# Performance work log

Hardware: AMD Instinct MI355X
Metric: run time of the kernel (lower is better)

## Reference

```python
import jax, jax.numpy as jnp
import numpy as np

N_NODES = 100000
N_EDGES = 3200000
HID = 32
N_LAYERS = 3
EDGE_DIM = 2
NODE_IN = 2          # [P, Q]
V_DIM = 2            # [V_mag, V_angle]
VH = V_DIM + HID     # 34, per-node feature fed to the GNN layer
MSG_IN = 2 * VH + EDGE_DIM   # 70
UPD_IN = VH + HID            # 66


def setup_inputs() -> dict:
    key = jax.random.key(0)
    ks = jax.random.split(key, 16)
    s = lambda *sh: 1.0 / np.sqrt(sh[-2]) if len(sh) >= 2 else 0.0
    inp = {
        "P_Q_inj": jax.random.normal(ks[0], (N_NODES, NODE_IN), dtype=jnp.float32),
        "senders": jax.random.randint(ks[1], (N_EDGES,), 0, N_NODES, dtype=jnp.int32),
        "receivers": jax.random.randint(ks[2], (N_EDGES,), 0, N_NODES, dtype=jnp.int32),
        "edge_features": jax.random.normal(ks[3], (N_EDGES, EDGE_DIM), dtype=jnp.float32),
        "edge_mask": jax.random.uniform(ks[4], (N_EDGES,), dtype=jnp.float32),
        # input embedding Dense(hidden_dim)
        "W_in": jax.random.normal(ks[5], (NODE_IN, HID), dtype=jnp.float32) * s(NODE_IN, HID),
        "b_in": jnp.zeros((HID,), dtype=jnp.float32),
        # per-layer params (flax compact loop -> distinct params per layer), stacked on axis 0
        "W_msg": jax.random.normal(ks[6], (N_LAYERS, MSG_IN, HID), dtype=jnp.float32) * s(MSG_IN, HID),
        "b_msg": jnp.zeros((N_LAYERS, HID), dtype=jnp.float32),
        "W_upd": jax.random.normal(ks[7], (N_LAYERS, UPD_IN, HID), dtype=jnp.float32) * s(UPD_IN, HID),
        "b_upd": jnp.zeros((N_LAYERS, HID), dtype=jnp.float32),
        "W_delta": jax.random.normal(ks[8], (N_LAYERS, HID, V_DIM), dtype=jnp.float32) * s(HID, V_DIM),
        "b_delta": jnp.zeros((N_LAYERS, V_DIM), dtype=jnp.float32),
    }
    return inp


def _layer(v, senders, receivers, edge_features, edge_mask, W_msg, b_msg, W_upd, b_upd):
    # v: [N, VH] node features. Gather sender/receiver feats, edge-wise MLP message,
    # soft mask, scatter-sum to receivers, then dense node update.
    msg_in = jnp.concatenate([v[senders], v[receivers], edge_features], axis=-1)  # [E, 70]
    m = jax.nn.relu(msg_in @ W_msg + b_msg)                                       # [E, H]
    m = m * edge_mask[:, None]
    agg = jax.ops.segment_sum(m, receivers, num_segments=v.shape[0])              # [N, H]
    v_out = jnp.concatenate([v, agg], axis=-1) @ W_upd + b_upd                    # [N, H]
    return v_out


def reference(P_Q_inj, senders, receivers, edge_features, edge_mask,
              W_in, b_in, W_msg, b_msg, W_upd, b_upd, W_delta, b_delta):
    V_pred = jnp.zeros_like(P_Q_inj).at[:, 0].set(1.0)   # [N, 2]
    h = P_Q_inj @ W_in + b_in                            # [N, H]
    for l in range(N_LAYERS):
        v_input = jnp.concatenate([V_pred, h], axis=-1)  # [N, 34]
        v_out = _layer(v_input, senders, receivers, edge_features, edge_mask,
                       W_msg[l], b_msg[l], W_upd[l], b_upd[l])
        h = jax.nn.relu(v_out)
        delta_V = h @ W_delta[l] + b_delta[l]
        V_pred = V_pred + delta_V
    return V_pred
```

## Files before the change

kernel.cpp:

```cpp
#include <hip/hip_runtime.h>
#include <hip/hip_fp16.h>

#define NN 100000
#define NE 3200000
#define NB 1563
#define NBLK ((NN + 255) / 256)
#define CHUNK 8192
#define NCH 391
#define CAP 4096
#define NKEY 8192

typedef float f32x4 __attribute__((ext_vector_type(4)));
typedef unsigned int u32x4 __attribute__((ext_vector_type(4)));

__device__ __forceinline__ float2 h2f2(unsigned int u) {
  __half2 h;
  *reinterpret_cast<unsigned int*>(&h) = u;
  return __half22float2(h);
}
__device__ __forceinline__ unsigned int f2h2(float x, float y) {
  __half2 h = __floats2half2_rn(x, y);
  return *reinterpret_cast<unsigned int*>(&h);
}


__global__ __launch_bounds__(1024) void k_hist(const int* __restrict__ recv, int* __restrict__ histmat) {
  __shared__ int h[NB];
  int t = threadIdx.x, c = blockIdx.x;
  for (int i = t; i < NB; i += 1024) h[i] = 0;
  __syncthreads();
  int start = c * CHUNK;
  int end = min(start + CHUNK, NE);
  for (int i = start + t; i < end; i += 1024)
    atomicAdd(&h[__builtin_nontemporal_load(recv + i) >> 6], 1);
  __syncthreads();
  for (int i = t; i < NB; i += 1024) histmat[c * NB + i] = h[i];
}


__global__ __launch_bounds__(256) void k_scanA(const int* __restrict__ histmat, int* __restrict__ total) {
  int b = blockIdx.x * 256 + threadIdx.x;
  if (b >= NB) return;
  int s = 0;
#pragma unroll 4
  for (int c = 0; c < NCH; c++) s += histmat[c * NB + b];
  total[b] = s;
}


__global__ __launch_bounds__(256) void k_scanB(const int* __restrict__ total, int* __restrict__ boff) {
  __shared__ int ps[256];
  int t = threadIdx.x;
  const int PER = (NB + 255) / 256;
  int v[PER];
  int s = 0;
#pragma unroll
  for (int k = 0; k < PER; k++) {
    int i = t * PER + k;
    v[k] = (i < NB) ? total[i] : 0;
    s += v[k];
  }
  ps[t] = s;
  __syncthreads();
  for (int o = 1; o < 256; o <<= 1) {
    int x = (t >= o) ? ps[t - o] : 0;
    __syncthreads();
    ps[t] += x;
    __syncthreads();
  }
  int run = (t > 0) ? ps[t - 1] : 0;
#pragma unroll
  for (int k = 0; k < PER; k++) {
    int i = t * PER + k;
    if (i < NB) {
      boff[i] = run;
      run += v[k];
    }
  }
  if (t == 255) boff[NB] = ps[255];
}


__global__ __launch_bounds__(256) void k_scanC(int* __restrict__ histmat, const int* __restrict__ boff) {
  int b = blockIdx.x * 256 + threadIdx.x;
  if (b >= NB) return;
  int run = boff[b];
#pragma unroll 4
  for (int c = 0; c < NCH; c++) {
    int v = histmat[c * NB + b];
    histmat[c * NB + b] = run;
    run += v;
  }
}


__global__ __launch_bounds__(1024) void k_scat(const int* __restrict__ send, const int* __restrict__ recv,
                                               const float2* __restrict__ ef, const float* __restrict__ mask,
                                               const int* __restrict__ boffc, float4* __restrict__ sorted) {
  __shared__ float4 stg[CHUNK];
  __shared__ unsigned short bkt[CHUNK];
  __shared__ int ofs[NB];
  __shared__ int cur[NB];
  __shared__ int wsum[16];
  int t = threadIdx.x, c = blockIdx.x;
  int start = c * CHUNK;
  int end = min(start + CHUNK, NE);
  int len = end - start;
  for (int i = t; i < NB; i += 1024) cur[i] = 0;
  __syncthreads();
  for (int i = start + t; i < end; i += 1024)
    atomicAdd(&cur[__builtin_nontemporal_load(recv + i) >> 6], 1);
  __syncthreads();
  int v0 = (2 * t < NB) ? cur[2 * t] : 0;
  int v1 = (2 * t + 1 < NB) ? cur[2 * t + 1] : 0;
  int s = v0 + v1;
  int lane = t & 63, wid = t >> 6;
  for (int o = 1; o < 64; o <<= 1) {
    int x = __shfl_up(s, o);
    if (lane >= o) s += x;
  }
  if (lane == 63) wsum[wid] = s;
  __syncthreads();
  if (wid == 0) {
    int ws = (lane < 16) ? wsum[lane] : 0;
    for (int o = 1; o < 16; o <<= 1) {
      int x = __shfl_up(ws, o);
      if (lane >= o) ws += x;
    }
    if (lane < 16) wsum[lane] = ws;
  }
  __syncthreads();
  int excl = s - v0 - v1 + ((wid > 0) ? wsum[wid - 1] : 0);
  __syncthreads();
  if (2 * t < NB) {
    cur[2 * t] = excl;
    ofs[2 * t] = boffc[c * NB + 2 * t] - excl;
  }
  if (2 * t + 1 < NB) {
    cur[2 * t + 1] = excl + v0;
    ofs[2 * t + 1] = boffc[c * NB + 2 * t + 1] - (excl + v0);
  }
  __syncthreads();
  for (int i = start + t; i < end; i += 1024) {
    int r = recv[i];
    int b = r >> 6;
    int p = atomicAdd(&cur[b], 1);
    float2 e2 = ef[i];
    float4 vv;
    vv.x = __int_as_float((send[i] << 6) | (r & 63));
    vv.y = e2.x;
    vv.z = e2.y;
    vv.w = mask[i];
    stg[p] = vv;
    bkt[p] = (unsigned short)b;
  }
  __syncthreads();
  for (int p = t; p < len; p += 1024) {
    int b = bkt[p];
    sorted[ofs[b] + p] = stg[p];
  }
}


__global__ __launch_bounds__(256) void k_bsort(const int* __restrict__ boff, float4* __restrict__ sorted,
                                               int* __restrict__ row_off) {
  __shared__ int cnt[NKEY];
  __shared__ int part[256];
  __shared__ float4 stg[CAP];
  int t = threadIdx.x, b = blockIdx.x;
  int base = boff[b], end = boff[b + 1];
  int Eb = end - base;
  int n0 = b * 64;
  for (int i = t; i < NKEY; i += 256) cnt[i] = 0;
  __syncthreads();
  for (int e = base + t; e < end; e += 256) {
    int pk = __float_as_int(sorted[e].x);
    int key = ((pk & 63) << 7) | (pk >> 16);
    atomicAdd(&cnt[key], 1);
  }
  __syncthreads();
  int s = 0;
#pragma unroll
  for (int k = 0; k < 32; k++) s += cnt[t * 32 + k];
  part[t] = s;
  __syncthreads();
  for (int o = 1; o < 256; o <<= 1) {
    int x = (t >= o) ? part[t - o] : 0;
    __syncthreads();
    part[t] += x;
    __syncthreads();
  }
  int run = part[t] - s;
#pragma unroll
  for (int k = 0; k < 32; k++) {
    int c = cnt[t * 32 + k];
    cnt[t * 32 + k] = run;
    run += c;
  }
  __syncthreads();
  if (t < 64) {
    int n = n0 + t;
    if (n < NN) row_off[n] = base + cnt[t << 7];
  }
  if (b == NB - 1 && t == 0) row_off[NN] = end;
  __syncthreads();
  for (int e = base + t; e < end; e += 256) {
    float4 r = sorted[e];
    int pk = __float_as_int(r.x);
    int key = ((pk & 63) << 7) | (pk >> 16);
    int p = atomicAdd(&cnt[key], 1);
    stg[p] = r;
  }
  __syncthreads();
  for (int i = t; i < Eb; i += 256) sorted[base + i] = stg[i];
}


__global__ __launch_bounds__(256) void k_init(const float2* __restrict__ PQ,
                                              const float* __restrict__ Win, const float* __restrict__ bin,
                                              const float* __restrict__ Wm, const float* __restrict__ bm,
                                              float* __restrict__ h, __half* __restrict__ a,
                                              float* __restrict__ bp, float2* __restrict__ Vp) {
  int n = blockIdx.x * 256 + threadIdx.x;
  if (n >= NN) return;
  float2 pq = PQ[n];
  float hh[32];
#pragma unroll
  for (int j = 0; j < 32; j++) hh[j] = fmaf(pq.x, Win[j], fmaf(pq.y, Win[32 + j], bin[j]));
  float4* h4 = (float4*)(h + (size_t)n * 32);
#pragma unroll
  for (int j = 0; j < 8; j++) h4[j] = make_float4(hh[4*j], hh[4*j+1], hh[4*j+2], hh[4*j+3]);
  Vp[n] = make_float2(1.0f, 0.0f);
  float av[32], bv[32];
#pragma unroll
  for (int j = 0; j < 32; j++) { av[j] = Wm[j]; bv[j] = Wm[34 * 32 + j] + bm[j]; }
#pragma unroll 1
  for (int k = 0; k < 32; k++) {
    float hk = hh[k];
#pragma unroll
    for (int j = 0; j < 32; j++) {
      av[j] = fmaf(hk, Wm[(2 + k) * 32 + j], av[j]);
      bv[j] = fmaf(hk, Wm[(36 + k) * 32 + j], bv[j]);
    }
  }
  u32x4* dst = (u32x4*)(a + (size_t)n * 32);
#pragma unroll
  for (int g = 0; g < 4; g++) {
    u32x4 p;
    p.x = f2h2(av[g*8+0], av[g*8+1]);
    p.y = f2h2(av[g*8+2], av[g*8+3]);
    p.z = f2h2(av[g*8+4], av[g*8+5]);
    p.w = f2h2(av[g*8+6], av[g*8+7]);
    dst[g] = p;
  }
  float4* b4 = (float4*)(bp + (size_t)n * 32);
#pragma unroll
  for (int j = 0; j < 8; j++) b4[j] = make_float4(bv[4*j], bv[4*j+1], bv[4*j+2], bv[4*j+3]);
}


__global__ __launch_bounds__(256) void k_edge(const __half* __restrict__ a, const float* __restrict__ bp,
                                              const int* __restrict__ row_off, const f32x4* __restrict__ sorted,
                                              const float* __restrict__ Wm, float* __restrict__ agg) {
  int t = threadIdx.x;
  int n = blockIdx.x * 64 + (t >> 2);
  if (n >= NN) return;
  int ch = (t & 3) * 8;
  const float* wr = Wm + 68 * 32 + ch;
  float w0[8], w1[8];
#pragma unroll
  for (int j = 0; j < 8; j++) { w0[j] = wr[j]; w1[j] = wr[32 + j]; }
  const float4 bna = *(const float4*)(bp + (size_t)n * 32 + ch);
  const float4 bnb = *(const float4*)(bp + (size_t)n * 32 + ch + 4);
  float bn[8] = {bna.x, bna.y, bna.z, bna.w, bnb.x, bnb.y, bnb.z, bnb.w};
  float acc[8] = {0.f, 0.f, 0.f, 0.f, 0.f, 0.f, 0.f, 0.f};
  const __half* abase = a + ch;
  int e0 = row_off[n], e1 = row_off[n + 1];
  f32x4 r0 = {0,0,0,0}, r1 = {0,0,0,0}, r2 = {0,0,0,0};
  u32x4 gA = {0,0,0,0}, gB = {0,0,0,0};
  if (e0 < e1)     r0 = __builtin_nontemporal_load(sorted + e0);
  if (e0 + 1 < e1) r1 = __builtin_nontemporal_load(sorted + e0 + 1);
  if (e0 + 2 < e1) r2 = __builtin_nontemporal_load(sorted + e0 + 2);
  if (e0 < e1)     gA = *(const u32x4*)(abase + (size_t)(__float_as_int(r0.x) >> 6) * 32);
  if (e0 + 1 < e1) gB = *(const u32x4*)(abase + (size_t)(__float_as_int(r1.x) >> 6) * 32);
  for (int e = e0; e < e1; ++e) {
    f32x4 rc = r0;
    u32x4 q = gA;
    r0 = r1; r1 = r2; gA = gB;
    if (e + 3 < e1) r2 = __builtin_nontemporal_load(sorted + e + 3);
    if (e + 2 < e1)
      gB = *(const u32x4*)(abase + (size_t)(__float_as_int(r1.x) >> 6) * 32);
    float c0 = rc.y, c1 = rc.z, mk = rc.w;
    float2 f0 = h2f2(q.x), f1 = h2f2(q.y), f2 = h2f2(q.z), f3 = h2f2(q.w);
    float av[8] = {f0.x, f0.y, f1.x, f1.y, f2.x, f2.y, f3.x, f3.y};
#pragma unroll
    for (int j = 0; j < 8; j++)
      acc[j] = fmaf(fmaxf(av[j] + fmaf(c0, w0[j], fmaf(c1, w1[j], bn[j])), 0.f), mk, acc[j]);
  }
  float* gp = agg + (size_t)n * 32 + ch;
  *(float4*)gp       = make_float4(acc[0], acc[1], acc[2], acc[3]);
  *(float4*)(gp + 4) = make_float4(acc[4], acc[5], acc[6], acc[7]);
}


__global__ __launch_bounds__(256) void k_node(const float* __restrict__ agg,
                                              const float* __restrict__ Wu, const float* __restrict__ bu,
                                              const float* __restrict__ Wd, const float* __restrict__ bd,
                                              const float* __restrict__ Wm, const float* __restrict__ bm,
                                              float* __restrict__ h, __half* __restrict__ a,
                                              float* __restrict__ bp, float2* __restrict__ Vp,
                                              float2* __restrict__ out, int last) {
  int n = blockIdx.x * 256 + threadIdx.x;
  if (n >= NN) return;
  float2 vp = Vp[n];
  float v0 = vp.x, v1 = vp.y;
  float hh[32], ag[32];
  const float4* h4 = (const float4*)(h + (size_t)n * 32);
  const float4* g4 = (const float4*)(agg + (size_t)n * 32);
#pragma unroll
  for (int jj = 0; jj < 8; jj++) {
    float4 x = h4[jj];
    hh[4*jj] = x.x; hh[4*jj+1] = x.y; hh[4*jj+2] = x.z; hh[4*jj+3] = x.w;
    float4 y = g4[jj];
    ag[4*jj] = y.x; ag[4*jj+1] = y.y; ag[4*jj+2] = y.z; ag[4*jj+3] = y.w;
  }
  float vo[32];
#pragma unroll
  for (int j = 0; j < 32; j++) vo[j] = fmaf(v0, Wu[j], fmaf(v1, Wu[32 + j], bu[j]));
#pragma unroll 1
  for (int k = 0; k < 32; k++) {
    float hk = hh[k], ak = ag[k];
#pragma unroll
    for (int j = 0; j < 32; j++) {
      vo[j] = fmaf(hk, Wu[(2 + k) * 32 + j], vo[j]);
      vo[j] = fmaf(ak, Wu[(34 + k) * 32 + j], vo[j]);
    }
  }
#pragma unroll
  for (int j = 0; j < 32; j++) hh[j] = fmaxf(vo[j], 0.0f);
  float d0 = bd[0], d1 = bd[1];
#pragma unroll 1
  for (int k = 0; k < 32; k++) {
    d0 = fmaf(hh[k], Wd[2 * k], d0);
    d1 = fmaf(hh[k], Wd[2 * k + 1], d1);
  }
  v0 += d0;
  v1 += d1;
  if (last) {
    out[n] = make_float2(v0, v1);
    return;
  }
  Vp[n] = make_float2(v0, v1);
  float4* hw4 = (float4*)(h + (size_t)n * 32);
#pragma unroll
  for (int jj = 0; jj < 8; jj++) hw4[jj] = make_float4(hh[4*jj], hh[4*jj+1], hh[4*jj+2], hh[4*jj+3]);
  float av[32], bv[32];
#pragma unroll
  for (int j = 0; j < 32; j++) {
    av[j] = fmaf(v0, Wm[j], v1 * Wm[32 + j]);
    bv[j] = fmaf(v0, Wm[34 * 32 + j], fmaf(v1, Wm[35 * 32 + j], bm[j]));
  }
#pragma unroll 1
  for (int k = 0; k < 32; k++) {
    float hk = hh[k];
#pragma unroll
    for (int j = 0; j < 32; j++) {
      av[j] = fmaf(hk, Wm[(2 + k) * 32 + j], av[j]);
      bv[j] = fmaf(hk, Wm[(36 + k) * 32 + j], bv[j]);
    }
  }
  u32x4* dst = (u32x4*)(a + (size_t)n * 32);
#pragma unroll
  for (int g = 0; g < 4; g++) {
    u32x4 p;
    p.x = f2h2(av[g*8+0], av[g*8+1]);
    p.y = f2h2(av[g*8+2], av[g*8+3]);
    p.z = f2h2(av[g*8+4], av[g*8+5]);
    p.w = f2h2(av[g*8+6], av[g*8+7]);
    dst[g] = p;
  }
  float4* b4 = (float4*)(bp + (size_t)n * 32);
#pragma unroll
  for (int jj = 0; jj < 8; jj++) b4[jj] = make_float4(bv[4*jj], bv[4*jj+1], bv[4*jj+2], bv[4*jj+3]);
}


extern "C" void kernel_launch(void* const* d_in, const int* in_sizes, int n_in,
                              void* d_out, int out_size, void* d_ws, size_t ws_size,
                              hipStream_t stream) {
  const float* PQ   = (const float*)d_in[0];
  const int*   send = (const int*)d_in[1];
  const int*   recv = (const int*)d_in[2];
  const float* ef   = (const float*)d_in[3];
  const float* mask = (const float*)d_in[4];
  const float* Win  = (const float*)d_in[5];
  const float* bin  = (const float*)d_in[6];
  const float* Wmsg = (const float*)d_in[7];
  const float* bmsg = (const float*)d_in[8];
  const float* Wupd = (const float*)d_in[9];
  const float* bupd = (const float*)d_in[10];
  const float* Wdel = (const float*)d_in[11];
  const float* bdel = (const float*)d_in[12];
  float2* out = (float2*)d_out;

  char* w = (char*)d_ws;
  auto alloc = [&](size_t bytes) {
    char* p = w;
    w += (bytes + 255) & ~(size_t)255;
    return p;
  };
  float4* sorted = (float4*)alloc((size_t)NE * 16);
  int* histmat = (int*)alloc((size_t)NCH * NB * 4);
  int* total   = (int*)alloc((size_t)NB * 4);
  int* boff    = (int*)alloc(((size_t)NB + 1) * 4);
  int* row_off = (int*)alloc(((size_t)NN + 1) * 4);
  float* h    = (float*)alloc((size_t)NN * 32 * 4);
  __half* a   = (__half*)alloc((size_t)NN * 32 * 2);
  float* bp   = (float*)alloc((size_t)NN * 32 * 4);
  float* agg  = (float*)alloc((size_t)NN * 32 * 4);
  float2* Vp  = (float2*)alloc((size_t)NN * 8);

  k_hist<<<NCH, 1024, 0, stream>>>(recv, histmat);
  k_scanA<<<(NB + 255) / 256, 256, 0, stream>>>(histmat, total);
  k_scanB<<<1, 256, 0, stream>>>(total, boff);
  k_scanC<<<(NB + 255) / 256, 256, 0, stream>>>(histmat, boff);
  k_scat<<<NCH, 1024, 0, stream>>>(send, recv, (const float2*)ef, mask, histmat, sorted);
  k_bsort<<<NB, 256, 0, stream>>>(boff, sorted, row_off);

  k_init<<<NBLK, 256, 0, stream>>>((const float2*)PQ, Win, bin, Wmsg, bmsg, h, a, bp, Vp);

  for (int l = 0; l < 3; l++) {
    int last = (l == 2) ? 1 : 0;
    int lnext = (l + 1) % 3;
    k_edge<<<NB, 256, 0, stream>>>(a, bp, row_off, (const f32x4*)sorted, Wmsg + l * 70 * 32, agg);
    k_node<<<NBLK, 256, 0, stream>>>(agg, Wupd + l * 66 * 32, bupd + l * 32,
                                     Wdel + l * 64, bdel + l * 2,
                                     Wmsg + lnext * 70 * 32, bmsg + lnext * 32,
                                     h, a, bp, Vp, out, last);
  }
}
```

Baseline: 564.3 us.

## Split fp16 gather table into two channel halves processed by separate edge passes

Stores the per-node fp16 projected features as two planar halves of 16 channels each (32 bytes per node per half) instead of one 64-byte row. The edge kernel now runs twice per layer, and each pass gathers only one half, so the random-gather working set per pass is 3.2 MB rather than 6.4 MB and is more likely to stay cache-resident. The cost is reading the sorted edge stream and row offsets twice and doing twice the per-edge loop overhead for the same arithmetic.

```diff
diff --git a/kernel.cpp b/kernel.cpp
--- a/kernel.cpp
+++ b/kernel.cpp
@@ -12,6 +12,7 @@
 
 typedef float f32x4 __attribute__((ext_vector_type(4)));
 typedef unsigned int u32x4 __attribute__((ext_vector_type(4)));
+typedef unsigned int u32x2 __attribute__((ext_vector_type(2)));
 
 __device__ __forceinline__ float2 h2f2(unsigned int u) {
   __half2 h;
@@ -243,15 +244,16 @@
       bv[j] = fmaf(hk, Wm[(36 + k) * 32 + j], bv[j]);
     }
   }
-  u32x4* dst = (u32x4*)(a + (size_t)n * 32);
-#pragma unroll
-  for (int g = 0; g < 4; g++) {
-    u32x4 p;
-    p.x = f2h2(av[g*8+0], av[g*8+1]);
-    p.y = f2h2(av[g*8+2], av[g*8+3]);
-    p.z = f2h2(av[g*8+4], av[g*8+5]);
-    p.w = f2h2(av[g*8+6], av[g*8+7]);
-    dst[g] = p;
+#pragma unroll
+  for (int g = 0; g < 2; g++) {
+    u32x4 p0, p1;
+    p0.x = f2h2(av[g*16+0],  av[g*16+1]);  p0.y = f2h2(av[g*16+2],  av[g*16+3]);
+    p0.z = f2h2(av[g*16+4],  av[g*16+5]);  p0.w = f2h2(av[g*16+6],  av[g*16+7]);
+    p1.x = f2h2(av[g*16+8],  av[g*16+9]);  p1.y = f2h2(av[g*16+10], av[g*16+11]);
+    p1.z = f2h2(av[g*16+12], av[g*16+13]); p1.w = f2h2(av[g*16+14], av[g*16+15]);
+    u32x4* dst = (u32x4*)(a + ((size_t)g * NN + n) * 16);
+    dst[0] = p0;
+    dst[1] = p1;
   }
   float4* b4 = (float4*)(bp + (size_t)n * 32);
 #pragma unroll
@@ -261,45 +263,43 @@
 
 __global__ __launch_bounds__(256) void k_edge(const __half* __restrict__ a, const float* __restrict__ bp,
                                               const int* __restrict__ row_off, const f32x4* __restrict__ sorted,
-                                              const float* __restrict__ Wm, float* __restrict__ agg) {
+                                              const float* __restrict__ Wm, float* __restrict__ agg, int g) {
   int t = threadIdx.x;
   int n = blockIdx.x * 64 + (t >> 2);
   if (n >= NN) return;
-  int ch = (t & 3) * 8;
+  int cl = (t & 3) * 4;
+  int ch = g * 16 + cl;
   const float* wr = Wm + 68 * 32 + ch;
-  float w0[8], w1[8];
-#pragma unroll
-  for (int j = 0; j < 8; j++) { w0[j] = wr[j]; w1[j] = wr[32 + j]; }
-  const float4 bna = *(const float4*)(bp + (size_t)n * 32 + ch);
-  const float4 bnb = *(const float4*)(bp + (size_t)n * 32 + ch + 4);
-  float bn[8] = {bna.x, bna.y, bna.z, bna.w, bnb.x, bnb.y, bnb.z, bnb.w};
-  float acc[8] = {0.f, 0.f, 0.f, 0.f, 0.f, 0.f, 0.f, 0.f};
-  const __half* abase = a + ch;
+  float w0[4], w1[4];
+#pragma unroll
+  for (int j = 0; j < 4; j++) { w0[j] = wr[j]; w1[j] = wr[32 + j]; }
+  const float4 bnv = *(const float4*)(bp + (size_t)n * 32 + ch);
+  float bn[4] = {bnv.x, bnv.y, bnv.z, bnv.w};
+  float acc[4] = {0.f, 0.f, 0.f, 0.f};
+  const __half* abase = a + (size_t)g * NN * 16 + cl;
   int e0 = row_off[n], e1 = row_off[n + 1];
   f32x4 r0 = {0,0,0,0}, r1 = {0,0,0,0}, r2 = {0,0,0,0};
-  u32x4 gA = {0,0,0,0}, gB = {0,0,0,0};
+  u32x2 gA = {0, 0}, gB = {0, 0};
   if (e0 < e1)     r0 = __builtin_nontemporal_load(sorted + e0);
   if (e0 + 1 < e1) r1 = __builtin_nontemporal_load(sorted + e0 + 1);
   if (e0 + 2 < e1) r2 = __builtin_nontemporal_load(sorted + e0 + 2);
-  if (e0 < e1)     gA = *(const u32x4*)(abase + (size_t)(__float_as_int(r0.x) >> 6) * 32);
-  if (e0 + 1 < e1) gB = *(const u32x4*)(abase + (size_t)(__float_as_int(r1.x) >> 6) * 32);
+  if (e0 < e1)     gA = *(const u32x2*)(abase + (size_t)(__float_as_int(r0.x) >> 6) * 16);
+  if (e0 + 1 < e1) gB = *(const u32x2*)(abase + (size_t)(__float_as_int(r1.x) >> 6) * 16);
   for (int e = e0; e < e1; ++e) {
     f32x4 rc = r0;
-    u32x4 q = gA;
+    u32x2 q = gA;
     r0 = r1; r1 = r2; gA = gB;
     if (e + 3 < e1) r2 = __builtin_nontemporal_load(sorted + e + 3);
     if (e + 2 < e1)
-      gB = *(const u32x4*)(abase + (size_t)(__float_as_int(r1.x) >> 6) * 32);
+      gB = *(const u32x2*)(abase + (size_t)(__float_as_int(r1.x) >> 6) * 16);
     float c0 = rc.y, c1 = rc.z, mk = rc.w;
-    float2 f0 = h2f2(q.x), f1 = h2f2(q.y), f2 = h2f2(q.z), f3 = h2f2(q.w);
-    float av[8] = {f0.x, f0.y, f1.x, f1.y, f2.x, f2.y, f3.x, f3.y};
-#pragma unroll
-    for (int j = 0; j < 8; j++)
+    float2 f0 = h2f2(q.x), f1 = h2f2(q.y);
+    float av[4] = {f0.x, f0.y, f1.x, f1.y};
+#pragma unroll
+    for (int j = 0; j < 4; j++)
       acc[j] = fmaf(fmaxf(av[j] + fmaf(c0, w0[j], fmaf(c1, w1[j], bn[j])), 0.f), mk, acc[j]);
   }
-  float* gp = agg + (size_t)n * 32 + ch;
-  *(float4*)gp       = make_float4(acc[0], acc[1], acc[2], acc[3]);
-  *(float4*)(gp + 4) = make_float4(acc[4], acc[5], acc[6], acc[7]);
+  *(float4*)(agg + (size_t)n * 32 + ch) = make_float4(acc[0], acc[1], acc[2], acc[3]);
 }
 
 
@@ -369,15 +369,16 @@
       bv[j] = fmaf(hk, Wm[(36 + k) * 32 + j], bv[j]);
     }
   }
-  u32x4* dst = (u32x4*)(a + (size_t)n * 32);
-#pragma unroll
-  for (int g = 0; g < 4; g++) {
-    u32x4 p;
-    p.x = f2h2(av[g*8+0], av[g*8+1]);
-    p.y = f2h2(av[g*8+2], av[g*8+3]);
-    p.z = f2h2(av[g*8+4], av[g*8+5]);
-    p.w = f2h2(av[g*8+6], av[g*8+7]);
-    dst[g] = p;
+#pragma unroll
+  for (int g = 0; g < 2; g++) {
+    u32x4 p0, p1;
+    p0.x = f2h2(av[g*16+0],  av[g*16+1]);  p0.y = f2h2(av[g*16+2],  av[g*16+3]);
+    p0.z = f2h2(av[g*16+4],  av[g*16+5]);  p0.w = f2h2(av[g*16+6],  av[g*16+7]);
+    p1.x = f2h2(av[g*16+8],  av[g*16+9]);  p1.y = f2h2(av[g*16+10], av[g*16+11]);
+    p1.z = f2h2(av[g*16+12], av[g*16+13]); p1.w = f2h2(av[g*16+14], av[g*16+15]);
+    u32x4* dst = (u32x4*)(a + ((size_t)g * NN + n) * 16);
+    dst[0] = p0;
+    dst[1] = p1;
   }
   float4* b4 = (float4*)(bp + (size_t)n * 32);
 #pragma unroll
@@ -432,7 +433,8 @@
   for (int l = 0; l < 3; l++) {
     int last = (l == 2) ? 1 : 0;
     int lnext = (l + 1) % 3;
-    k_edge<<<NB, 256, 0, stream>>>(a, bp, row_off, (const f32x4*)sorted, Wmsg + l * 70 * 32, agg);
+    k_edge<<<NB, 256, 0, stream>>>(a, bp, row_off, (const f32x4*)sorted, Wmsg + l * 70 * 32, agg, 0);
+    k_edge<<<NB, 256, 0, stream>>>(a, bp, row_off, (const f32x4*)sorted, Wmsg + l * 70 * 32, agg, 1);
     k_node<<<NBLK, 256, 0, stream>>>(agg, Wupd + l * 66 * 32, bupd + l * 32,
                                      Wdel + l * 64, bdel + l * 2,
                                      Wmsg + lnext * 70 * 32, bmsg + lnext * 32,
```

Result: slower. 774.8 us (+37.3%).
